# Performance work log

Hardware: AMD Instinct MI355X
Metric: run time of the kernel (lower is better)

Reference implementation:

```python
import jax, jax.numpy as jnp
import numpy as np

N_HEAD = 8
LN_EPS = 1e-5


def _layernorm(x, w, b):
    mu = jnp.mean(x, axis=-1, keepdims=True)
    var = jnp.var(x, axis=-1, keepdims=True)
    return (x - mu) * jax.lax.rsqrt(var + LN_EPS) * w + b


def setup_inputs() -> dict:
    key = jax.random.key(0)
    ks = jax.random.split(key, 8)
    B, T, D, L, V, F = 4, 768, 512, 6, 50304, 2048
    s = 0.02
    return {
        "idx": jax.random.randint(ks[0], (B, T), 0, V),
        "wte": jax.random.normal(ks[1], (V, D), jnp.float32) * s,
        "wpe": jax.random.normal(ks[2], (T, D), jnp.float32) * s,
        "c_attn_w": jax.random.normal(ks[3], (L, 3 * D, D), jnp.float32) * s,
        "c_attn_b": jnp.zeros((L, 3 * D), jnp.float32),
        "c_proj_w": jax.random.normal(ks[4], (L, D, D), jnp.float32) * s,
        "c_proj_b": jnp.zeros((L, D), jnp.float32),
        "fc_w": jax.random.normal(ks[5], (L, F, D), jnp.float32) * s,
        "fc_b": jnp.zeros((L, F), jnp.float32),
        "fc2_w": jax.random.normal(ks[6], (L, D, F), jnp.float32) * s,
        "fc2_b": jnp.zeros((L, D), jnp.float32),
        "ln1_w": jnp.ones((L, D), jnp.float32),
        "ln1_b": jnp.zeros((L, D), jnp.float32),
        "ln2_w": jnp.ones((L, D), jnp.float32),
        "ln2_b": jnp.zeros((L, D), jnp.float32),
        "lnf_w": jnp.ones((D,), jnp.float32),
        "lnf_b": jnp.zeros((D,), jnp.float32),
    }


def _forward(idx, wte, wpe, c_attn_w, c_attn_b, c_proj_w, c_proj_b,
             fc_w, fc_b, fc2_w, fc2_b, ln1_w, ln1_b, ln2_w, ln2_b,
             lnf_w, lnf_b):
    B, T = idx.shape
    D = wte.shape[1]
    hd = D // N_HEAD
    causal = jnp.tril(jnp.ones((T, T), bool))  # [T,T]

    x = wte[idx] + wpe[:T]  # [B,T,D]; dropout is identity in eval

    def block(x, p):
        (aw, ab, pw, pb, fw, fb, f2w, f2b, l1w, l1b, l2w, l2b) = p
        # --- causal self-attention ---
        qkv = x @ aw.T + ab  # [B,T,3D]
        q, k, v = jnp.split(qkv, 3, axis=-1)
        q = q.reshape(B, T, N_HEAD, hd)
        k = k.reshape(B, T, N_HEAD, hd)
        v = v.reshape(B, T, N_HEAD, hd)
        att = jnp.einsum('bqhd,bkhd->bhqk', q, k) * (1.0 / np.sqrt(hd))
        att = jnp.where(causal, att, -jnp.inf)
        att = jax.nn.softmax(att, axis=-1)
        y = jnp.einsum('bhqk,bkhd->bqhd', att, v).reshape(B, T, D)
        y = y @ pw.T + pb
        x = _layernorm(x + y, l1w, l1b)  # post-norm as in source
        # --- feed-forward ---
        h = jax.nn.relu(x @ fw.T + fb)
        h = h @ f2w.T + f2b
        x = _layernorm(x + h, l2w, l2b)
        return x, None

    params = (c_attn_w, c_attn_b, c_proj_w, c_proj_b, fc_w, fc_b,
              fc2_w, fc2_b, ln1_w, ln1_b, ln2_w, ln2_b)
    x, _ = jax.lax.scan(block, x, params)
    x = _layernorm(x, lnf_w, lnf_b)
    logits = x @ wte.T  # tied head, no bias
    return logits


def reference(idx, wte, wpe, c_attn_w, c_attn_b, c_proj_w, c_proj_b,
              fc_w, fc_b, fc2_w, fc2_b, ln1_w, ln1_b, ln2_w, ln2_b,
              lnf_w, lnf_b):
    return _forward(idx, wte, wpe, c_attn_w, c_attn_b, c_proj_w, c_proj_b,
                    fc_w, fc_b, fc2_w, fc2_b, ln1_w, ln1_b, ln2_w, ln2_b,
                    lnf_w, lnf_b)
```

## Files before the change

### kernel.cpp

```cpp
#include <hip/hip_runtime.h>
#include <hip/hip_bf16.h>

#define AS1 __attribute__((address_space(1)))
#define AS3 __attribute__((address_space(3)))

typedef __attribute__((ext_vector_type(8))) short short8;
typedef __attribute__((ext_vector_type(4))) float f32x4;

constexpr int BB = 4, TT = 768, DDIM = 512, LL = 6, VV = 50304, FF = 2048;
constexpr int MM = BB * TT;

__device__ inline unsigned short f2b(float f) {
  union { float f; unsigned u; } a; a.f = f;
  unsigned u = a.u;
  return (unsigned short)((u + 0x7FFFu + ((u >> 16) & 1u)) >> 16);
}
__device__ inline float b2f(unsigned short u) {
  union { unsigned u; float f; } a; a.u = ((unsigned)u) << 16; return a.f;
}

constexpr size_t CW0 = (size_t)VV * DDIM;
constexpr size_t CW1 = CW0 + (size_t)LL * 3 * DDIM * DDIM;
constexpr size_t CW2 = CW1 + (size_t)LL * DDIM * DDIM;
constexpr size_t CW3 = CW2 + (size_t)LL * FF * DDIM;
constexpr size_t CW4 = CW3 + (size_t)LL * DDIM * FF;

__global__ void cvt_all(const float* __restrict__ wte, const float* __restrict__ aw,
                        const float* __restrict__ pw, const float* __restrict__ fw,
                        const float* __restrict__ f2w, ushort* __restrict__ out) {
  size_t i = ((size_t)blockIdx.x * 256 + threadIdx.x) * 4;
  if (i >= CW4) return;
  const float* src; size_t base;
  if (i < CW0)      { src = wte; base = 0; }
  else if (i < CW1) { src = aw;  base = CW0; }
  else if (i < CW2) { src = pw;  base = CW1; }
  else if (i < CW3) { src = fw;  base = CW2; }
  else              { src = f2w; base = CW3; }
  float4 v = *(const float4*)(src + (i - base));
  ushort4 o = { f2b(v.x), f2b(v.y), f2b(v.z), f2b(v.w) };
  *(ushort4*)(out + i) = o;
}

__global__ void embed_kernel(const int* __restrict__ idx, const float* __restrict__ wte,
                             const float* __restrict__ wpe, float* __restrict__ x,
                             ushort* __restrict__ xb) {
  int row = blockIdx.x;
  int t = row % TT;
  int tok = idx[row];
  int c = threadIdx.x * 4;
  float4 a = *(const float4*)(wte + (size_t)tok * DDIM + c);
  float4 p = *(const float4*)(wpe + (size_t)t * DDIM + c);
  a.x += p.x; a.y += p.y; a.z += p.z; a.w += p.w;
  *(float4*)(x + (size_t)row * DDIM + c) = a;
  ushort4 o = { f2b(a.x), f2b(a.y), f2b(a.z), f2b(a.w) };
  *(ushort4*)(xb + (size_t)row * DDIM + c) = o;
}

template <int RELU, int OUTBF16, int BM, int BN, int SWZ>
__global__ __launch_bounds__(256) void gemm_bt(
    const ushort* __restrict__ A, const ushort* __restrict__ Bw,
    const float* __restrict__ bias, void* __restrict__ Cv, int Ndim, int K) {
  constexpr int MI = BM / 32, NJ = BN / 32;
  __shared__ ushort sA[2][BM * 32];
  __shared__ ushort sB[2][BN * 32];
  const int tid = threadIdx.x;
  const int wid = tid >> 6, lane = tid & 63;
  int m0, n0;
  if (SWZ) {
    constexpr int MT = MM / BM;
    int id = blockIdx.x;
    int v = (id >> 3) + (id & 7) * ((int)gridDim.x >> 3);
    m0 = (v % MT) * BM;
    n0 = (v / MT) * BN;
  } else {
    m0 = blockIdx.y * BM;
    n0 = blockIdx.x * BN;
  }
  const int wm = (wid >> 1) * (BM / 2), wn = (wid & 1) * (BN / 2);

  f32x4 zero = {0.f, 0.f, 0.f, 0.f};
  f32x4 acc[MI][NJ];
#pragma unroll
  for (int i = 0; i < MI; i++)
#pragma unroll
    for (int j = 0; j < NJ; j++) acc[i][j] = zero;

  const int r4 = tid >> 2;
  const int c8 = (tid & 3) * 8;
  const ushort* gA = A + (size_t)(m0 + r4) * K + c8;
  const ushort* gB = Bw + (size_t)(n0 + r4) * K + c8;
  const size_t K64 = (size_t)64 * K;

  const int fr = lane & 15;
  const int fk = (lane >> 4) * 8;

  auto stage = [&](int buf, int kk) {
    const ushort* a0 = gA + kk * 32;
    const ushort* b0 = gB + kk * 32;
    ushort* dA = &sA[buf][0] + wid * 512;
    ushort* dB = &sB[buf][0] + wid * 512;
#pragma unroll
    for (int i = 0; i < BM / 64; i++)
      __builtin_amdgcn_global_load_lds((const AS1 void*)(a0 + (size_t)i * K64),
                                       (AS3 void*)(dA + i * 2048), 16, 0, 0);
#pragma unroll
    for (int i = 0; i < BN / 64; i++)
      __builtin_amdgcn_global_load_lds((const AS1 void*)(b0 + (size_t)i * K64),
                                       (AS3 void*)(dB + i * 2048), 16, 0, 0);
  };

  const int nK = K >> 5;
  stage(0, 0);
  __syncthreads();
  int buf = 0;
  for (int kk = 0; kk < nK; ++kk) {
    if (kk + 1 < nK) stage(buf ^ 1, kk + 1);
    const ushort* pa0 = &sA[buf][0] + (wm + fr) * 32 + fk;
    const ushort* pb0 = &sB[buf][0] + (wn + fr) * 32 + fk;
    short8 af[MI], bf[NJ];
#pragma unroll
    for (int i = 0; i < MI; i++) af[i] = *(const short8*)(pa0 + i * 16 * 32);
#pragma unroll
    for (int j = 0; j < NJ; j++) bf[j] = *(const short8*)(pb0 + j * 16 * 32);
#pragma unroll
    for (int i = 0; i < MI; i++)
#pragma unroll
      for (int j = 0; j < NJ; j++)
        acc[i][j] = __builtin_amdgcn_mfma_f32_16x16x32_bf16(af[i], bf[j], acc[i][j], 0, 0, 0);
    __syncthreads();
    buf ^= 1;
  }

  const int cr = (lane >> 4) * 4;
  const int cc = lane & 15;
#pragma unroll
  for (int j = 0; j < NJ; j++) {
    const int gcol = n0 + wn + j * 16 + cc;
    const float bv = bias ? bias[gcol] : 0.0f;
#pragma unroll
    for (int i = 0; i < MI; i++) {
      const int grow = m0 + wm + i * 16 + cr;
#pragma unroll
      for (int rr = 0; rr < 4; ++rr) {
        float v = acc[i][j][rr] + bv;
        if (RELU) v = fmaxf(v, 0.0f);
        if (OUTBF16)
          ((ushort*)Cv)[(size_t)(grow + rr) * Ndim + gcol] = f2b(v);
        else
          ((float*)Cv)[(size_t)(grow + rr) * Ndim + gcol] = v;
      }
    }
  }
}

__device__ inline short8 lds_swz_read(const ushort* base, int row, int elem) {
  return *(const short8*)((const char*)base + row * 128 + ((elem * 2) ^ ((row & 7) << 4)));
}

__global__ __launch_bounds__(256) void attn_mfma(const ushort* __restrict__ qkv,
                                                 ushort* __restrict__ yb) {
  __shared__ ushort sK[64 * 64];
  __shared__ ushort sVT[64 * 64];
  __shared__ ushort sP[4 * 16 * 64];
  const int tid = threadIdx.x;
  const int wid = tid >> 6, lane = tid & 63;
  const int qt = blockIdx.x;
  const int b = blockIdx.y >> 3, h = blockIdx.y & 7;
  const int q0 = qt * 64;
  const int qw = q0 + wid * 16;

  const int fr = lane & 15;
  const int fk = (lane >> 4) * 8;
  ushort* sPw = sP + wid * 16 * 64;

  short8 qf[2];
  {
    const ushort* qp = qkv + (size_t)(b * TT + qw + fr) * 1536 + h * 64;
    qf[0] = *(const short8*)(qp + fk);
    qf[1] = *(const short8*)(qp + 32 + fk);
  }

  const int r4 = tid >> 2;
  const int c32 = (tid & 3) * 16;

  f32x4 zero = {0.f, 0.f, 0.f, 0.f};
  f32x4 acc[4] = {zero, zero, zero, zero};
  float mrow[4] = {-INFINITY, -INFINITY, -INFINITY, -INFINITY};
  float lrow[4] = {0.f, 0.f, 0.f, 0.f};

  for (int kt = 0; kt <= qt; ++kt) {
    __syncthreads();
    const int k0 = kt * 64;
    {
      const ushort* kp = qkv + (size_t)(b * TT + k0 + r4) * 1536 + 512 + h * 64 + c32;
      short8 kv0 = *(const short8*)kp;
      short8 kv1 = *(const short8*)(kp + 8);
      char* skb = (char*)sK + r4 * 128;
      *(short8*)(skb + ((c32 * 2) ^ ((r4 & 7) << 4))) = kv0;
      *(short8*)(skb + ((c32 * 2 + 16) ^ ((r4 & 7) << 4))) = kv1;
      const ushort* vp = kp + 512;
      short8 vv0 = *(const short8*)vp;
      short8 vv1 = *(const short8*)(vp + 8);
#pragma unroll
      for (int i = 0; i < 8; i++) {
        int d0 = c32 + i, d1 = c32 + 8 + i;
        *(ushort*)((char*)sVT + d0 * 128 + ((r4 * 2) ^ ((d0 & 7) << 4))) = (ushort)vv0[i];
        *(ushort*)((char*)sVT + d1 * 128 + ((r4 * 2) ^ ((d1 & 7) << 4))) = (ushort)vv1[i];
      }
    }
    __syncthreads();

    f32x4 sfr[4];
#pragma unroll
    for (int j = 0; j < 4; j++) {
      short8 kb0 = lds_swz_read(sK, j * 16 + fr, fk);
      short8 kb1 = lds_swz_read(sK, j * 16 + fr, 32 + fk);
      f32x4 s = __builtin_amdgcn_mfma_f32_16x16x32_bf16(qf[0], kb0, zero, 0, 0, 0);
      s = __builtin_amdgcn_mfma_f32_16x16x32_bf16(qf[1], kb1, s, 0, 0, 0);
      sfr[j] = s * 0.125f;
    }
    if (kt == qt) {
#pragma unroll
      for (int j = 0; j < 4; j++)
#pragma unroll
        for (int rr = 0; rr < 4; ++rr)
          if (j * 16 + fr > wid * 16 + (lane >> 4) * 4 + rr) sfr[j][rr] = -INFINITY;
    }

    float scl[4];
#pragma unroll
    for (int rr = 0; rr < 4; ++rr) {
      float t = fmaxf(fmaxf(sfr[0][rr], sfr[1][rr]), fmaxf(sfr[2][rr], sfr[3][rr]));
      t = fmaxf(t, __shfl_xor(t, 1));
      t = fmaxf(t, __shfl_xor(t, 2));
      t = fmaxf(t, __shfl_xor(t, 4));
      t = fmaxf(t, __shfl_xor(t, 8));
      const float mnew = fmaxf(mrow[rr], t);
      scl[rr] = __expf(mrow[rr] - mnew);
      mrow[rr] = mnew;
      float ps = 0.f;
#pragma unroll
      for (int j = 0; j < 4; j++) {
        float p = __expf(sfr[j][rr] - mnew);
        sfr[j][rr] = p;
        ps += p;
      }
      ps += __shfl_xor(ps, 1);
      ps += __shfl_xor(ps, 2);
      ps += __shfl_xor(ps, 4);
      ps += __shfl_xor(ps, 8);
      lrow[rr] = lrow[rr] * scl[rr] + ps;
    }

#pragma unroll
    for (int j = 0; j < 4; j++)
#pragma unroll
      for (int rr = 0; rr < 4; ++rr) {
        int q = (lane >> 4) * 4 + rr, k = j * 16 + fr;
        *(ushort*)((char*)sPw + q * 128 + ((k * 2) ^ ((q & 7) << 4))) = f2b(sfr[j][rr]);
      }

#pragma unroll
    for (int f = 0; f < 4; f++)
#pragma unroll
      for (int rr = 0; rr < 4; ++rr) acc[f][rr] *= scl[rr];

    short8 pa0 = lds_swz_read(sPw, fr, fk);
    short8 pa1 = lds_swz_read(sPw, fr, 32 + fk);
#pragma unroll
    for (int f = 0; f < 4; f++) {
      short8 vb0 = lds_swz_read(sVT, f * 16 + fr, fk);
      short8 vb1 = lds_swz_read(sVT, f * 16 + fr, 32 + fk);
      acc[f] = __builtin_amdgcn_mfma_f32_16x16x32_bf16(pa0, vb0, acc[f], 0, 0, 0);
      acc[f] = __builtin_amdgcn_mfma_f32_16x16x32_bf16(pa1, vb1, acc[f], 0, 0, 0);
    }
  }

#pragma unroll
  for (int rr = 0; rr < 4; ++rr) {
    const float inv = 1.0f / lrow[rr];
    const int token = b * TT + qw + (lane >> 4) * 4 + rr;
    ushort* yp = yb + (size_t)token * DDIM + h * 64 + fr;
#pragma unroll
    for (int f = 0; f < 4; f++) yp[f * 16] = f2b(acc[f][rr] * inv);
  }
}

__global__ __launch_bounds__(256) void add_ln(const float* __restrict__ x,
                                              const float* __restrict__ y,
                                              const float* __restrict__ w,
                                              const float* __restrict__ bb,
                                              float* __restrict__ xo,
                                              ushort* __restrict__ xb) {
  const int row = blockIdx.x * 4 + (threadIdx.x >> 6);
  const int lane = threadIdx.x & 63;
  const size_t base = (size_t)row * DDIM + lane * 8;
  f32x4 a0 = *(const f32x4*)(x + base);
  f32x4 a1 = *(const f32x4*)(x + base + 4);
  if (y) {
    a0 += *(const f32x4*)(y + base);
    a1 += *(const f32x4*)(y + base + 4);
  }
  float s = (a0[0] + a0[1] + a0[2] + a0[3]) + (a1[0] + a1[1] + a1[2] + a1[3]);
  f32x4 q0 = a0 * a0, q1 = a1 * a1;
  float ss = (q0[0] + q0[1] + q0[2] + q0[3]) + (q1[0] + q1[1] + q1[2] + q1[3]);
#pragma unroll
  for (int o = 1; o < 64; o <<= 1) {
    s += __shfl_xor(s, o);
    ss += __shfl_xor(ss, o);
  }
  const float mu = s * (1.0f / DDIM);
  const float var = ss * (1.0f / DDIM) - mu * mu;
  const float rs = rsqrtf(var + 1e-5f);
  const int c = lane * 8;
  f32x4 w0 = *(const f32x4*)(w + c), w1 = *(const f32x4*)(w + c + 4);
  f32x4 b0 = *(const f32x4*)(bb + c), b1 = *(const f32x4*)(bb + c + 4);
  f32x4 o0 = (a0 - mu) * rs * w0 + b0;
  f32x4 o1 = (a1 - mu) * rs * w1 + b1;
  *(f32x4*)(xo + base) = o0;
  *(f32x4*)(xo + base + 4) = o1;
  ushort4 u0 = { f2b(o0[0]), f2b(o0[1]), f2b(o0[2]), f2b(o0[3]) };
  ushort4 u1 = { f2b(o1[0]), f2b(o1[1]), f2b(o1[2]), f2b(o1[3]) };
  *(ushort4*)(xb + base) = u0;
  *(ushort4*)(xb + base + 4) = u1;
}

extern "C" void kernel_launch(void* const* d_in, const int* in_sizes, int n_in,
                              void* d_out, int out_size, void* d_ws, size_t ws_size,
                              hipStream_t stream) {
  const int*   idx  = (const int*)d_in[0];
  const float* wte  = (const float*)d_in[1];
  const float* wpe  = (const float*)d_in[2];
  const float* aw   = (const float*)d_in[3];
  const float* ab   = (const float*)d_in[4];
  const float* pw   = (const float*)d_in[5];
  const float* pb   = (const float*)d_in[6];
  const float* fw   = (const float*)d_in[7];
  const float* fb   = (const float*)d_in[8];
  const float* f2w  = (const float*)d_in[9];
  const float* f2bi = (const float*)d_in[10];
  const float* l1w  = (const float*)d_in[11];
  const float* l1b  = (const float*)d_in[12];
  const float* l2w  = (const float*)d_in[13];
  const float* l2b  = (const float*)d_in[14];
  const float* lnfw = (const float*)d_in[15];
  const float* lnfb = (const float*)d_in[16];

  char* ws = (char*)d_ws;
  size_t off = 0;
  auto take = [&](size_t bytes) -> void* {
    void* p = ws + off;
    off += (bytes + 255) & ~(size_t)255;
    return p;
  };
  ushort* wte_b = (ushort*)take((size_t)VV * DDIM * 2);
  ushort* aw_b  = (ushort*)take((size_t)LL * 3 * DDIM * DDIM * 2);
  ushort* pw_b  = (ushort*)take((size_t)LL * DDIM * DDIM * 2);
  ushort* fw_b  = (ushort*)take((size_t)LL * FF * DDIM * 2);
  ushort* f2w_b = (ushort*)take((size_t)LL * DDIM * FF * 2);
  float*  x     = (float*)take((size_t)MM * DDIM * 4);
  ushort* xb    = (ushort*)take((size_t)MM * DDIM * 2);
  ushort* qkv_b = (ushort*)take((size_t)MM * 3 * DDIM * 2);
  ushort* yb    = (ushort*)take((size_t)MM * DDIM * 2);
  float*  tmp   = (float*)take((size_t)MM * DDIM * 4);
  ushort* hb    = (ushort*)take((size_t)MM * FF * 2);

  cvt_all<<<dim3((unsigned)(CW4 / 4 / 256)), dim3(256), 0, stream>>>(
      wte, aw, pw, fw, f2w, wte_b);

  embed_kernel<<<dim3(MM), dim3(128), 0, stream>>>(idx, wte, wpe, x, xb);

  for (int l = 0; l < LL; ++l) {
    gemm_bt<0, 1, 128, 64, 0><<<dim3(24, 24), dim3(256), 0, stream>>>(
        xb, aw_b + (size_t)l * 3 * DDIM * DDIM, ab + (size_t)l * 3 * DDIM, qkv_b, 3 * DDIM, DDIM);
    attn_mfma<<<dim3(TT / 64, BB * 8), dim3(256), 0, stream>>>(qkv_b, yb);
    gemm_bt<0, 0, 64, 64, 0><<<dim3(8, 48), dim3(256), 0, stream>>>(
        yb, pw_b + (size_t)l * DDIM * DDIM, pb + (size_t)l * DDIM, tmp, DDIM, DDIM);
    add_ln<<<dim3(MM / 4), dim3(256), 0, stream>>>(
        x, tmp, l1w + (size_t)l * DDIM, l1b + (size_t)l * DDIM, x, xb);
    gemm_bt<1, 1, 128, 64, 0><<<dim3(32, 24), dim3(256), 0, stream>>>(
        xb, fw_b + (size_t)l * FF * DDIM, fb + (size_t)l * FF, hb, FF, DDIM);
    gemm_bt<0, 0, 64, 64, 0><<<dim3(8, 48), dim3(256), 0, stream>>>(
        hb, f2w_b + (size_t)l * DDIM * FF, f2bi + (size_t)l * DDIM, tmp, DDIM, FF);
    add_ln<<<dim3(MM / 4), dim3(256), 0, stream>>>(
        x, tmp, l2w + (size_t)l * DDIM, l2b + (size_t)l * DDIM, x, xb);
  }
  add_ln<<<dim3(MM / 4), dim3(256), 0, stream>>>(x, nullptr, lnfw, lnfb, x, xb);

  gemm_bt<0, 0, 128, 128, 1><<<dim3((VV / 128) * 24), dim3(256), 0, stream>>>(
      xb, wte_b, nullptr, (float*)d_out, VV, DDIM);
}
```

Before: 1.028 ms.

## Use K=64 swizzled-LDS GEMM with split-K for projection GEMMs

```diff
diff --git a/kernel.cpp b/kernel.cpp
--- a/kernel.cpp
+++ b/kernel.cpp
@@ -56,26 +56,18 @@
   *(ushort4*)(xb + (size_t)row * DDIM + c) = o;
 }
 
-template <int RELU, int OUTBF16, int BM, int BN, int SWZ>
-__global__ __launch_bounds__(256) void gemm_bt(
+template <int RELU, int OUTBF16, int BM, int BN, int SPLITK>
+__global__ __launch_bounds__(256) void gemm_bt64(
     const ushort* __restrict__ A, const ushort* __restrict__ Bw,
     const float* __restrict__ bias, void* __restrict__ Cv, int Ndim, int K) {
   constexpr int MI = BM / 32, NJ = BN / 32;
-  __shared__ ushort sA[2][BM * 32];
-  __shared__ ushort sB[2][BN * 32];
+  __shared__ ushort sA[2][BM * 64];
+  __shared__ ushort sB[2][BN * 64];
   const int tid = threadIdx.x;
   const int wid = tid >> 6, lane = tid & 63;
-  int m0, n0;
-  if (SWZ) {
-    constexpr int MT = MM / BM;
-    int id = blockIdx.x;
-    int v = (id >> 3) + (id & 7) * ((int)gridDim.x >> 3);
-    m0 = (v % MT) * BM;
-    n0 = (v / MT) * BN;
-  } else {
-    m0 = blockIdx.y * BM;
-    n0 = blockIdx.x * BN;
-  }
+  const int m0 = blockIdx.y * BM, n0 = blockIdx.x * BN;
+  const int kchunk = K / SPLITK;
+  const int ks0 = (SPLITK > 1) ? blockIdx.z * kchunk : 0;
   const int wm = (wid >> 1) * (BM / 2), wn = (wid & 1) * (BN / 2);
 
   f32x4 zero = {0.f, 0.f, 0.f, 0.f};
@@ -84,6 +76,103 @@
   for (int i = 0; i < MI; i++)
 #pragma unroll
     for (int j = 0; j < NJ; j++) acc[i][j] = zero;
+
+  const int r = tid >> 3;
+  const int cg = ((tid & 7) ^ (r & 7)) * 8;
+  const ushort* gA = A + (size_t)(m0 + r) * K + ks0 + cg;
+  const ushort* gB = Bw + (size_t)(n0 + r) * K + ks0 + cg;
+
+  auto stage = [&](int buf, int kk) {
+    const ushort* a0 = gA + kk * 64;
+    const ushort* b0 = gB + kk * 64;
+    ushort* dA = &sA[buf][0] + wid * 512;
+    ushort* dB = &sB[buf][0] + wid * 512;
+#pragma unroll
+    for (int p = 0; p < BM / 32; p++)
+      __builtin_amdgcn_global_load_lds((const AS1 void*)(a0 + (size_t)p * 32 * K),
+                                       (AS3 void*)(dA + p * 2048), 16, 0, 0);
+#pragma unroll
+    for (int p = 0; p < BN / 32; p++)
+      __builtin_amdgcn_global_load_lds((const AS1 void*)(b0 + (size_t)p * 32 * K),
+                                       (AS3 void*)(dB + p * 2048), 16, 0, 0);
+  };
+
+  const int fr = lane & 15;
+  const int fk = (lane >> 4) * 8;
+  auto ldfrag = [&](const ushort* s, int rowbase, int sub) -> short8 {
+    const int row = rowbase + fr;
+    const int off = row * 128 + ((sub * 64 + fk * 2) ^ ((fr & 7) << 4));
+    return *(const short8*)((const char*)s + off);
+  };
+
+  const int nK = kchunk >> 6;
+  stage(0, 0);
+  __syncthreads();
+  int buf = 0;
+  for (int kk = 0; kk < nK; ++kk) {
+    if (kk + 1 < nK) stage(buf ^ 1, kk + 1);
+    short8 af[MI][2], bf[NJ][2];
+#pragma unroll
+    for (int i = 0; i < MI; i++)
+#pragma unroll
+      for (int s = 0; s < 2; s++) af[i][s] = ldfrag(&sA[buf][0], wm + i * 16, s);
+#pragma unroll
+    for (int j = 0; j < NJ; j++)
+#pragma unroll
+      for (int s = 0; s < 2; s++) bf[j][s] = ldfrag(&sB[buf][0], wn + j * 16, s);
+#pragma unroll
+    for (int i = 0; i < MI; i++)
+#pragma unroll
+      for (int j = 0; j < NJ; j++)
+#pragma unroll
+        for (int s = 0; s < 2; s++)
+          acc[i][j] = __builtin_amdgcn_mfma_f32_16x16x32_bf16(af[i][s], bf[j][s], acc[i][j], 0, 0, 0);
+    __syncthreads();
+    buf ^= 1;
+  }
+
+  const int cr = (lane >> 4) * 4;
+  const int cc = lane & 15;
+  float* Cf = (float*)Cv + (SPLITK > 1 ? (size_t)blockIdx.z * MM * Ndim : 0);
+#pragma unroll
+  for (int j = 0; j < NJ; j++) {
+    const int gcol = n0 + wn + j * 16 + cc;
+    const float bv = (bias && (SPLITK == 1 || blockIdx.z == 0)) ? bias[gcol] : 0.0f;
+#pragma unroll
+    for (int i = 0; i < MI; i++) {
+      const int grow = m0 + wm + i * 16 + cr;
+#pragma unroll
+      for (int rr = 0; rr < 4; ++rr) {
+        float v = acc[i][j][rr] + bv;
+        if (RELU) v = fmaxf(v, 0.0f);
+        if (OUTBF16)
+          ((ushort*)Cv)[(size_t)(grow + rr) * Ndim + gcol] = f2b(v);
+        else
+          Cf[(size_t)(grow + rr) * Ndim + gcol] = v;
+      }
+    }
+  }
+}
+
+__global__ __launch_bounds__(256) void gemm_head(
+    const ushort* __restrict__ A, const ushort* __restrict__ Bw,
+    float* __restrict__ Cv, int Ndim, int K) {
+  __shared__ ushort sA[2][128 * 32];
+  __shared__ ushort sB[2][128 * 32];
+  const int tid = threadIdx.x;
+  const int wid = tid >> 6, lane = tid & 63;
+  int id = blockIdx.x;
+  int v = (id >> 3) + (id & 7) * ((int)gridDim.x >> 3);
+  const int m0 = (v % 24) * 128;
+  const int n0 = (v / 24) * 128;
+  const int wm = (wid >> 1) * 64, wn = (wid & 1) * 64;
+
+  f32x4 zero = {0.f, 0.f, 0.f, 0.f};
+  f32x4 acc[4][4];
+#pragma unroll
+  for (int i = 0; i < 4; i++)
+#pragma unroll
+    for (int j = 0; j < 4; j++) acc[i][j] = zero;
 
   const int r4 = tid >> 2;
   const int c8 = (tid & 3) * 8;
@@ -91,24 +180,23 @@
   const ushort* gB = Bw + (size_t)(n0 + r4) * K + c8;
   const size_t K64 = (size_t)64 * K;
 
-  const int fr = lane & 15;
-  const int fk = (lane >> 4) * 8;
-
   auto stage = [&](int buf, int kk) {
     const ushort* a0 = gA + kk * 32;
     const ushort* b0 = gB + kk * 32;
     ushort* dA = &sA[buf][0] + wid * 512;
     ushort* dB = &sB[buf][0] + wid * 512;
 #pragma unroll
-    for (int i = 0; i < BM / 64; i++)
+    for (int i = 0; i < 2; i++)
       __builtin_amdgcn_global_load_lds((const AS1 void*)(a0 + (size_t)i * K64),
                                        (AS3 void*)(dA + i * 2048), 16, 0, 0);
 #pragma unroll
-    for (int i = 0; i < BN / 64; i++)
+    for (int i = 0; i < 2; i++)
       __builtin_amdgcn_global_load_lds((const AS1 void*)(b0 + (size_t)i * K64),
                                        (AS3 void*)(dB + i * 2048), 16, 0, 0);
   };
 
+  const int fr = lane & 15;
+  const int fk = (lane >> 4) * 8;
   const int nK = K >> 5;
   stage(0, 0);
   __syncthreads();
@@ -117,15 +205,15 @@
     if (kk + 1 < nK) stage(buf ^ 1, kk + 1);
     const ushort* pa0 = &sA[buf][0] + (wm + fr) * 32 + fk;
     const ushort* pb0 = &sB[buf][0] + (wn + fr) * 32 + fk;
-    short8 af[MI], bf[NJ];
-#pragma unroll
-    for (int i = 0; i < MI; i++) af[i] = *(const short8*)(pa0 + i * 16 * 32);
-#pragma unroll
-    for (int j = 0; j < NJ; j++) bf[j] = *(const short8*)(pb0 + j * 16 * 32);
-#pragma unroll
-    for (int i = 0; i < MI; i++)
-#pragma unroll
-      for (int j = 0; j < NJ; j++)
+    short8 af[4], bf[4];
+#pragma unroll
+    for (int i = 0; i < 4; i++) af[i] = *(const short8*)(pa0 + i * 16 * 32);
+#pragma unroll
+    for (int j = 0; j < 4; j++) bf[j] = *(const short8*)(pb0 + j * 16 * 32);
+#pragma unroll
+    for (int i = 0; i < 4; i++)
+#pragma unroll
+      for (int j = 0; j < 4; j++)
         acc[i][j] = __builtin_amdgcn_mfma_f32_16x16x32_bf16(af[i], bf[j], acc[i][j], 0, 0, 0);
     __syncthreads();
     buf ^= 1;
@@ -134,21 +222,14 @@
   const int cr = (lane >> 4) * 4;
   const int cc = lane & 15;
 #pragma unroll
-  for (int j = 0; j < NJ; j++) {
+  for (int j = 0; j < 4; j++) {
     const int gcol = n0 + wn + j * 16 + cc;
-    const float bv = bias ? bias[gcol] : 0.0f;
-#pragma unroll
-    for (int i = 0; i < MI; i++) {
+#pragma unroll
+    for (int i = 0; i < 4; i++) {
       const int grow = m0 + wm + i * 16 + cr;
 #pragma unroll
-      for (int rr = 0; rr < 4; ++rr) {
-        float v = acc[i][j][rr] + bv;
-        if (RELU) v = fmaxf(v, 0.0f);
-        if (OUTBF16)
-          ((ushort*)Cv)[(size_t)(grow + rr) * Ndim + gcol] = f2b(v);
-        else
-          ((float*)Cv)[(size_t)(grow + rr) * Ndim + gcol] = v;
-      }
+      for (int rr = 0; rr < 4; ++rr)
+        Cv[(size_t)(grow + rr) * Ndim + gcol] = acc[i][j][rr];
     }
   }
 }
@@ -286,6 +367,7 @@
   }
 }
 
+template <int S>
 __global__ __launch_bounds__(256) void add_ln(const float* __restrict__ x,
                                               const float* __restrict__ y,
                                               const float* __restrict__ w,
@@ -297,19 +379,20 @@
   const size_t base = (size_t)row * DDIM + lane * 8;
   f32x4 a0 = *(const f32x4*)(x + base);
   f32x4 a1 = *(const f32x4*)(x + base + 4);
-  if (y) {
-    a0 += *(const f32x4*)(y + base);
-    a1 += *(const f32x4*)(y + base + 4);
-  }
-  float s = (a0[0] + a0[1] + a0[2] + a0[3]) + (a1[0] + a1[1] + a1[2] + a1[3]);
+#pragma unroll
+  for (int s = 0; s < S; ++s) {
+    a0 += *(const f32x4*)(y + (size_t)s * MM * DDIM + base);
+    a1 += *(const f32x4*)(y + (size_t)s * MM * DDIM + base + 4);
+  }
+  float sm = (a0[0] + a0[1] + a0[2] + a0[3]) + (a1[0] + a1[1] + a1[2] + a1[3]);
   f32x4 q0 = a0 * a0, q1 = a1 * a1;
   float ss = (q0[0] + q0[1] + q0[2] + q0[3]) + (q1[0] + q1[1] + q1[2] + q1[3]);
 #pragma unroll
   for (int o = 1; o < 64; o <<= 1) {
-    s += __shfl_xor(s, o);
+    sm += __shfl_xor(sm, o);
     ss += __shfl_xor(ss, o);
   }
-  const float mu = s * (1.0f / DDIM);
+  const float mu = sm * (1.0f / DDIM);
   const float var = ss * (1.0f / DDIM) - mu * mu;
   const float rs = rsqrtf(var + 1e-5f);
   const int c = lane * 8;
@@ -362,7 +445,7 @@
   ushort* xb    = (ushort*)take((size_t)MM * DDIM * 2);
   ushort* qkv_b = (ushort*)take((size_t)MM * 3 * DDIM * 2);
   ushort* yb    = (ushort*)take((size_t)MM * DDIM * 2);
-  float*  tmp   = (float*)take((size_t)MM * DDIM * 4);
+  float*  tmp   = (float*)take((size_t)4 * MM * DDIM * 4);
   ushort* hb    = (ushort*)take((size_t)MM * FF * 2);
 
   cvt_all<<<dim3((unsigned)(CW4 / 4 / 256)), dim3(256), 0, stream>>>(
@@ -371,22 +454,22 @@
   embed_kernel<<<dim3(MM), dim3(128), 0, stream>>>(idx, wte, wpe, x, xb);
 
   for (int l = 0; l < LL; ++l) {
-    gemm_bt<0, 1, 128, 64, 0><<<dim3(24, 24), dim3(256), 0, stream>>>(
+    gemm_bt64<0, 1, 128, 64, 1><<<dim3(24, 24), dim3(256), 0, stream>>>(
         xb, aw_b + (size_t)l * 3 * DDIM * DDIM, ab + (size_t)l * 3 * DDIM, qkv_b, 3 * DDIM, DDIM);
     attn_mfma<<<dim3(TT / 64, BB * 8), dim3(256), 0, stream>>>(qkv_b, yb);
-    gemm_bt<0, 0, 64, 64, 0><<<dim3(8, 48), dim3(256), 0, stream>>>(
+    gemm_bt64<0, 0, 64, 64, 2><<<dim3(8, 48, 2), dim3(256), 0, stream>>>(
         yb, pw_b + (size_t)l * DDIM * DDIM, pb + (size_t)l * DDIM, tmp, DDIM, DDIM);
-    add_ln<<<dim3(MM / 4), dim3(256), 0, stream>>>(
+    add_ln<2><<<dim3(MM / 4), dim3(256), 0, stream>>>(
         x, tmp, l1w + (size_t)l * DDIM, l1b + (size_t)l * DDIM, x, xb);
-    gemm_bt<1, 1, 128, 64, 0><<<dim3(32, 24), dim3(256), 0, stream>>>(
+    gemm_bt64<1, 1, 128, 64, 1><<<dim3(32, 24), dim3(256), 0, stream>>>(
         xb, fw_b + (size_t)l * FF * DDIM, fb + (size_t)l * FF, hb, FF, DDIM);
-    gemm_bt<0, 0, 64, 64, 0><<<dim3(8, 48), dim3(256), 0, stream>>>(
+    gemm_bt64<0, 0, 64, 64, 4><<<dim3(8, 48, 4), dim3(256), 0, stream>>>(
         hb, f2w_b + (size_t)l * DDIM * FF, f2bi + (size_t)l * DDIM, tmp, DDIM, FF);
-    add_ln<<<dim3(MM / 4), dim3(256), 0, stream>>>(
+    add_ln<4><<<dim3(MM / 4), dim3(256), 0, stream>>>(
         x, tmp, l2w + (size_t)l * DDIM, l2b + (size_t)l * DDIM, x, xb);
   }
-  add_ln<<<dim3(MM / 4), dim3(256), 0, stream>>>(x, nullptr, lnfw, lnfb, x, xb);
-
-  gemm_bt<0, 0, 128, 128, 1><<<dim3((VV / 128) * 24), dim3(256), 0, stream>>>(
-      xb, wte_b, nullptr, (float*)d_out, VV, DDIM);
-}
+  add_ln<0><<<dim3(MM / 4), dim3(256), 0, stream>>>(x, nullptr, lnfw, lnfb, x, xb);
+
+  gemm_head<<<dim3((VV / 128) * 24), dim3(256), 0, stream>>>(
+      xb, wte_b, (float*)d_out, VV, DDIM);
+}
```

After: 901.1 us. -12.3%, faster.

## Rewrite GEMM with triple-buffered K=64 pipeline, swizzled LDS, split-K and bf16 partials

Applied to the files above, without the earlier changes.

```diff
diff --git a/kernel.cpp b/kernel.cpp
--- a/kernel.cpp
+++ b/kernel.cpp
@@ -56,27 +56,36 @@
   *(ushort4*)(xb + (size_t)row * DDIM + c) = o;
 }
 
-template <int RELU, int OUTBF16, int BM, int BN, int SWZ>
-__global__ __launch_bounds__(256) void gemm_bt(
+template <int RELU, int OUTBF16, int BM, int BN, int SPLITK, int SWZ, int NT>
+__global__ __launch_bounds__(NT, 2) void gemm_pipe(
     const ushort* __restrict__ A, const ushort* __restrict__ Bw,
     const float* __restrict__ bias, void* __restrict__ Cv, int Ndim, int K) {
-  constexpr int MI = BM / 32, NJ = BN / 32;
-  __shared__ ushort sA[2][BM * 32];
-  __shared__ ushort sB[2][BN * 32];
+  constexpr int WM = (NT == 512) ? 4 : 2;
+  constexpr int WTM = BM / WM, WTN = BN / 2;
+  constexpr int MI = WTM / 16, NJ = WTN / 16;
+  constexpr int TILE = (BM + BN) * 64;
+  constexpr int RPI = NT / 8;
+  constexpr int LOADS = (BM + BN) / RPI;
+  __shared__ ushort sT[3][TILE];
+
   const int tid = threadIdx.x;
   const int wid = tid >> 6, lane = tid & 63;
   int m0, n0;
   if (SWZ) {
     constexpr int MT = MM / BM;
-    int id = blockIdx.x;
-    int v = (id >> 3) + (id & 7) * ((int)gridDim.x >> 3);
+    const int nwg = (int)gridDim.x;
+    const int q = nwg >> 3, rm = nwg & 7;
+    const int xcd = blockIdx.x & 7, pos = blockIdx.x >> 3;
+    const int v = (xcd < rm ? xcd * (q + 1) : rm * (q + 1) + (xcd - rm) * q) + pos;
     m0 = (v % MT) * BM;
     n0 = (v / MT) * BN;
   } else {
     m0 = blockIdx.y * BM;
     n0 = blockIdx.x * BN;
   }
-  const int wm = (wid >> 1) * (BM / 2), wn = (wid & 1) * (BN / 2);
+  const int kchunk = K / SPLITK;
+  const int ks0 = (SPLITK > 1) ? blockIdx.z * kchunk : 0;
+  const int wm = (wid >> 1) * WTM, wn = (wid & 1) * WTN;
 
   f32x4 zero = {0.f, 0.f, 0.f, 0.f};
   f32x4 acc[MI][NJ];
@@ -85,58 +94,86 @@
 #pragma unroll
     for (int j = 0; j < NJ; j++) acc[i][j] = zero;
 
-  const int r4 = tid >> 2;
-  const int c8 = (tid & 3) * 8;
-  const ushort* gA = A + (size_t)(m0 + r4) * K + c8;
-  const ushort* gB = Bw + (size_t)(n0 + r4) * K + c8;
-  const size_t K64 = (size_t)64 * K;
+  const int r = tid >> 3;
+  const int cg = ((tid & 7) ^ (r & 7)) * 8;
+  const ushort* gA = A + (size_t)(m0 + r) * K + ks0 + cg;
+  const ushort* gB = Bw + (size_t)(n0 + r) * K + ks0 + cg;
+
+  auto stage = [&](int buf, int t) {
+    const ushort* a0 = gA + t * 64;
+    const ushort* b0 = gB + t * 64;
+    ushort* dA = &sT[buf][0] + wid * 512;
+    ushort* dB = &sT[buf][BM * 64] + wid * 512;
+#pragma unroll
+    for (int p = 0; p < BM / RPI; p++)
+      __builtin_amdgcn_global_load_lds((const AS1 void*)(a0 + (size_t)p * RPI * K),
+                                       (AS3 void*)(dA + p * RPI * 64), 16, 0, 0);
+#pragma unroll
+    for (int p = 0; p < BN / RPI; p++)
+      __builtin_amdgcn_global_load_lds((const AS1 void*)(b0 + (size_t)p * RPI * K),
+                                       (AS3 void*)(dB + p * RPI * 64), 16, 0, 0);
+  };
 
   const int fr = lane & 15;
   const int fk = (lane >> 4) * 8;
-
-  auto stage = [&](int buf, int kk) {
-    const ushort* a0 = gA + kk * 32;
-    const ushort* b0 = gB + kk * 32;
-    ushort* dA = &sA[buf][0] + wid * 512;
-    ushort* dB = &sB[buf][0] + wid * 512;
-#pragma unroll
-    for (int i = 0; i < BM / 64; i++)
-      __builtin_amdgcn_global_load_lds((const AS1 void*)(a0 + (size_t)i * K64),
-                                       (AS3 void*)(dA + i * 2048), 16, 0, 0);
-#pragma unroll
-    for (int i = 0; i < BN / 64; i++)
-      __builtin_amdgcn_global_load_lds((const AS1 void*)(b0 + (size_t)i * K64),
-                                       (AS3 void*)(dB + i * 2048), 16, 0, 0);
+  auto ldfrag = [&](const char* base, int rowbase, int sub) -> short8 {
+    const int row = rowbase + fr;
+    const int off = row * 128 + ((sub * 64 + fk * 2) ^ ((fr & 7) << 4));
+    return *(const short8*)(base + off);
   };
 
-  const int nK = K >> 5;
+  const int nK = kchunk >> 6;
   stage(0, 0);
-  __syncthreads();
-  int buf = 0;
-  for (int kk = 0; kk < nK; ++kk) {
-    if (kk + 1 < nK) stage(buf ^ 1, kk + 1);
-    const ushort* pa0 = &sA[buf][0] + (wm + fr) * 32 + fk;
-    const ushort* pb0 = &sB[buf][0] + (wn + fr) * 32 + fk;
-    short8 af[MI], bf[NJ];
-#pragma unroll
-    for (int i = 0; i < MI; i++) af[i] = *(const short8*)(pa0 + i * 16 * 32);
-#pragma unroll
-    for (int j = 0; j < NJ; j++) bf[j] = *(const short8*)(pb0 + j * 16 * 32);
+  if (nK > 1) {
+    stage(1, 1);
+    asm volatile("s_waitcnt vmcnt(%0)" :: "i"(LOADS) : "memory");
+  } else {
+    asm volatile("s_waitcnt vmcnt(0)" ::: "memory");
+  }
+  __builtin_amdgcn_s_barrier();
+  __builtin_amdgcn_sched_barrier(0);
+
+  for (int t = 0; t < nK; ++t) {
+    if (t + 2 < nK) stage((t + 2) % 3, t + 2);
+    const char* bufA = (const char*)&sT[t % 3][0];
+    const char* bufB = bufA + BM * 128;
+    short8 af[MI][2], bf[NJ][2];
 #pragma unroll
     for (int i = 0; i < MI; i++)
 #pragma unroll
+      for (int s = 0; s < 2; s++) af[i][s] = ldfrag(bufA, wm + i * 16, s);
+#pragma unroll
+    for (int j = 0; j < NJ; j++)
+#pragma unroll
+      for (int s = 0; s < 2; s++) bf[j][s] = ldfrag(bufB, wn + j * 16, s);
+    __builtin_amdgcn_s_setprio(1);
+#pragma unroll
+    for (int i = 0; i < MI; i++)
+#pragma unroll
       for (int j = 0; j < NJ; j++)
-        acc[i][j] = __builtin_amdgcn_mfma_f32_16x16x32_bf16(af[i], bf[j], acc[i][j], 0, 0, 0);
-    __syncthreads();
-    buf ^= 1;
+#pragma unroll
+        for (int s = 0; s < 2; s++)
+          acc[i][j] = __builtin_amdgcn_mfma_f32_16x16x32_bf16(af[i][s], bf[j][s], acc[i][j], 0, 0, 0);
+    __builtin_amdgcn_s_setprio(0);
+    if (t + 1 < nK) {
+      if (t + 2 < nK)
+        asm volatile("s_waitcnt vmcnt(%0)" :: "i"(LOADS) : "memory");
+      else
+        asm volatile("s_waitcnt vmcnt(0)" ::: "memory");
+      __builtin_amdgcn_s_barrier();
+      __builtin_amdgcn_sched_barrier(0);
+    }
   }
 
   const int cr = (lane >> 4) * 4;
   const int cc = lane & 15;
+  const size_t zoff = (SPLITK > 1) ? (size_t)blockIdx.z * MM * Ndim : 0;
+  ushort* Cb = (ushort*)Cv + zoff;
+  float*  Cf = (float*)Cv + zoff;
 #pragma unroll
   for (int j = 0; j < NJ; j++) {
     const int gcol = n0 + wn + j * 16 + cc;
-    const float bv = bias ? bias[gcol] : 0.0f;
+    const float bv = (bias && (SPLITK == 1 || blockIdx.z == 0)) ? bias[gcol] : 0.0f;
 #pragma unroll
     for (int i = 0; i < MI; i++) {
       const int grow = m0 + wm + i * 16 + cr;
@@ -145,9 +182,9 @@
         float v = acc[i][j][rr] + bv;
         if (RELU) v = fmaxf(v, 0.0f);
         if (OUTBF16)
-          ((ushort*)Cv)[(size_t)(grow + rr) * Ndim + gcol] = f2b(v);
+          Cb[(size_t)(grow + rr) * Ndim + gcol] = f2b(v);
         else
-          ((float*)Cv)[(size_t)(grow + rr) * Ndim + gcol] = v;
+          Cf[(size_t)(grow + rr) * Ndim + gcol] = v;
       }
     }
   }
@@ -286,8 +323,9 @@
   }
 }
 
+template <int S>
 __global__ __launch_bounds__(256) void add_ln(const float* __restrict__ x,
-                                              const float* __restrict__ y,
+                                              const ushort* __restrict__ y,
                                               const float* __restrict__ w,
                                               const float* __restrict__ bb,
                                               float* __restrict__ xo,
@@ -297,19 +335,24 @@
   const size_t base = (size_t)row * DDIM + lane * 8;
   f32x4 a0 = *(const f32x4*)(x + base);
   f32x4 a1 = *(const f32x4*)(x + base + 4);
-  if (y) {
-    a0 += *(const f32x4*)(y + base);
-    a1 += *(const f32x4*)(y + base + 4);
-  }
-  float s = (a0[0] + a0[1] + a0[2] + a0[3]) + (a1[0] + a1[1] + a1[2] + a1[3]);
+#pragma unroll
+  for (int s = 0; s < S; ++s) {
+    short8 v = *(const short8*)(y + (size_t)s * MM * DDIM + base);
+    f32x4 p0 = { b2f((unsigned short)v[0]), b2f((unsigned short)v[1]),
+                 b2f((unsigned short)v[2]), b2f((unsigned short)v[3]) };
+    f32x4 p1 = { b2f((unsigned short)v[4]), b2f((unsigned short)v[5]),
+                 b2f((unsigned short)v[6]), b2f((unsigned short)v[7]) };
+    a0 += p0; a1 += p1;
+  }
+  float sm = (a0[0] + a0[1] + a0[2] + a0[3]) + (a1[0] + a1[1] + a1[2] + a1[3]);
   f32x4 q0 = a0 * a0, q1 = a1 * a1;
   float ss = (q0[0] + q0[1] + q0[2] + q0[3]) + (q1[0] + q1[1] + q1[2] + q1[3]);
 #pragma unroll
   for (int o = 1; o < 64; o <<= 1) {
-    s += __shfl_xor(s, o);
+    sm += __shfl_xor(sm, o);
     ss += __shfl_xor(ss, o);
   }
-  const float mu = s * (1.0f / DDIM);
+  const float mu = sm * (1.0f / DDIM);
   const float var = ss * (1.0f / DDIM) - mu * mu;
   const float rs = rsqrtf(var + 1e-5f);
   const int c = lane * 8;
@@ -362,7 +405,7 @@
   ushort* xb    = (ushort*)take((size_t)MM * DDIM * 2);
   ushort* qkv_b = (ushort*)take((size_t)MM * 3 * DDIM * 2);
   ushort* yb    = (ushort*)take((size_t)MM * DDIM * 2);
-  float*  tmp   = (float*)take((size_t)MM * DDIM * 4);
+  ushort* tmp_b = (ushort*)take((size_t)2 * MM * DDIM * 2);
   ushort* hb    = (ushort*)take((size_t)MM * FF * 2);
 
   cvt_all<<<dim3((unsigned)(CW4 / 4 / 256)), dim3(256), 0, stream>>>(
@@ -371,22 +414,22 @@
   embed_kernel<<<dim3(MM), dim3(128), 0, stream>>>(idx, wte, wpe, x, xb);
 
   for (int l = 0; l < LL; ++l) {
-    gemm_bt<0, 1, 128, 64, 0><<<dim3(24, 24), dim3(256), 0, stream>>>(
+    gemm_pipe<0, 1, 128, 64, 1, 0, 256><<<dim3(24, 24), dim3(256), 0, stream>>>(
         xb, aw_b + (size_t)l * 3 * DDIM * DDIM, ab + (size_t)l * 3 * DDIM, qkv_b, 3 * DDIM, DDIM);
     attn_mfma<<<dim3(TT / 64, BB * 8), dim3(256), 0, stream>>>(qkv_b, yb);
-    gemm_bt<0, 0, 64, 64, 0><<<dim3(8, 48), dim3(256), 0, stream>>>(
-        yb, pw_b + (size_t)l * DDIM * DDIM, pb + (size_t)l * DDIM, tmp, DDIM, DDIM);
-    add_ln<<<dim3(MM / 4), dim3(256), 0, stream>>>(
-        x, tmp, l1w + (size_t)l * DDIM, l1b + (size_t)l * DDIM, x, xb);
-    gemm_bt<1, 1, 128, 64, 0><<<dim3(32, 24), dim3(256), 0, stream>>>(
+    gemm_pipe<0, 1, 64, 64, 2, 0, 256><<<dim3(8, 48, 2), dim3(256), 0, stream>>>(
+        yb, pw_b + (size_t)l * DDIM * DDIM, pb + (size_t)l * DDIM, tmp_b, DDIM, DDIM);
+    add_ln<2><<<dim3(MM / 4), dim3(256), 0, stream>>>(
+        x, tmp_b, l1w + (size_t)l * DDIM, l1b + (size_t)l * DDIM, x, xb);
+    gemm_pipe<1, 1, 128, 64, 1, 0, 256><<<dim3(32, 24), dim3(256), 0, stream>>>(
         xb, fw_b + (size_t)l * FF * DDIM, fb + (size_t)l * FF, hb, FF, DDIM);
-    gemm_bt<0, 0, 64, 64, 0><<<dim3(8, 48), dim3(256), 0, stream>>>(
-        hb, f2w_b + (size_t)l * DDIM * FF, f2bi + (size_t)l * DDIM, tmp, DDIM, FF);
-    add_ln<<<dim3(MM / 4), dim3(256), 0, stream>>>(
-        x, tmp, l2w + (size_t)l * DDIM, l2b + (size_t)l * DDIM, x, xb);
-  }
-  add_ln<<<dim3(MM / 4), dim3(256), 0, stream>>>(x, nullptr, lnfw, lnfb, x, xb);
-
-  gemm_bt<0, 0, 128, 128, 1><<<dim3((VV / 128) * 24), dim3(256), 0, stream>>>(
+    gemm_pipe<0, 1, 64, 64, 2, 0, 256><<<dim3(8, 48, 2), dim3(256), 0, stream>>>(
+        hb, f2w_b + (size_t)l * DDIM * FF, f2bi + (size_t)l * DDIM, tmp_b, DDIM, FF);
+    add_ln<2><<<dim3(MM / 4), dim3(256), 0, stream>>>(
+        x, tmp_b, l2w + (size_t)l * DDIM, l2b + (size_t)l * DDIM, x, xb);
+  }
+  add_ln<0><<<dim3(MM / 4), dim3(256), 0, stream>>>(x, nullptr, lnfw, lnfb, x, xb);
+
+  gemm_pipe<0, 0, 256, 128, 1, 1, 512><<<dim3((MM / 256) * (VV / 128)), dim3(512), 0, stream>>>(
       xb, wte_b, nullptr, (float*)d_out, VV, DDIM);
 }
```

Result: faster. 906.4 us (-11.8%).
